# Kernel tuning notes

Hardware: AMD Instinct MI355X
Metric: run time of the kernel (lower is better)

## Reference

```python
import jax, jax.numpy as jnp
import numpy as np

N_NODES = 50000
N_RELS = 50
N_CLASSES = 40
EMB_DIM = 16
RP = 16
N_TRIPLES = 400000


def setup_inputs() -> dict:
    rng = np.random.default_rng(0)
    s = rng.integers(0, N_NODES, size=N_TRIPLES)
    r = rng.integers(0, N_RELS, size=N_TRIPLES)
    o = rng.integers(0, N_NODES, size=N_TRIPLES)
    # unique (s,o) pairs, as in torch.unique(pairs, dim=0, return_inverse=True)
    pairs = np.stack([s, o], axis=1)
    unique_pairs, inverse = np.unique(pairs, axis=0, return_inverse=True)
    nt = unique_pairs.shape[0]
    # relation_matrix COO (nt, num_rels), coalesced (duplicate (row,col) summed)
    keys = inverse.astype(np.int64) * N_RELS + r
    uk, counts = np.unique(keys, return_counts=True)
    rm_rows = (uk // N_RELS).astype(np.int32)
    rm_cols = (uk % N_RELS).astype(np.int32)
    rm_vals = counts.astype(np.float32)
    # hindices / vindices exactly as in __init__ (note o*rm / s*rm construction)
    s_u = unique_pairs[:, 0].astype(np.int64)
    o_u = unique_pairs[:, 1].astype(np.int64)
    rm = np.arange(RP, dtype=np.int64)[:, None]            # (rp, 1)
    h_rows = np.broadcast_to(s_u[None, :], (RP, nt)).reshape(-1).astype(np.int32)
    h_cols = (o_u[None, :] * rm).reshape(-1).astype(np.int32)
    v_rows = (s_u[None, :] * rm).reshape(-1).astype(np.int32)
    v_cols = np.broadcast_to(o_u[None, :], (RP, nt)).reshape(-1).astype(np.int32)
    # float params (xavier-like scale for weights, randn for rel emb, zero biases)
    key = jax.random.key(0)
    k1, k2, k3 = jax.random.split(key, 3)
    gain = np.sqrt(2.0)  # relu gain
    w1_std = gain * np.sqrt(2.0 / (N_NODES + EMB_DIM))
    w2_std = gain * np.sqrt(2.0 / (EMB_DIM + N_CLASSES))
    return {
        'rel_emb': jax.random.normal(k1, (N_RELS, RP), dtype=jnp.float32),
        'weights1': jax.random.normal(k2, (RP, N_NODES, EMB_DIM), dtype=jnp.float32) * w1_std,
        'weights2': jax.random.normal(k3, (RP, EMB_DIM, N_CLASSES), dtype=jnp.float32) * w2_std,
        'bias1': jnp.zeros((EMB_DIM,), dtype=jnp.float32),
        'bias2': jnp.zeros((N_CLASSES,), dtype=jnp.float32),
        'rm_rows': jnp.asarray(rm_rows),
        'rm_cols': jnp.asarray(rm_cols),
        'rm_vals': jnp.asarray(rm_vals),
        'h_rows': jnp.asarray(h_rows),
        'h_cols': jnp.asarray(h_cols),
        'v_rows': jnp.asarray(v_rows),
        'v_cols': jnp.asarray(v_cols),
    }


def reference(rel_emb, weights1, weights2, bias1, bias2,
              rm_rows, rm_cols, rm_vals, h_rows, h_cols, v_rows, v_cols):
    rp, n, e = weights1.shape
    nt = h_rows.shape[0] // rp
    # latents = sparse.mm(relation_matrix, relation_embeddings) -> (nt, rp)
    latents = jax.ops.segment_sum(rm_vals[:, None] * rel_emb[rm_cols], rm_rows,
                                  num_segments=nt)
    latents = jax.nn.softmax(latents, axis=1)
    lf = latents.T.reshape(-1)                              # (rp*nt,)
    # sum_sparse(hindices, lf, (n, n*rp), row=False): per-column sums, gathered
    colsum = jax.ops.segment_sum(lf, h_cols, num_segments=n * rp)
    ln = lf / colsum[h_cols]
    # spmm(hindices, ln, (n, n*rp), weights1_flat) -> (n, e)
    w1f = weights1.reshape(rp * n, e)
    h = jax.ops.segment_sum(ln[:, None] * w1f[h_cols], h_rows, num_segments=n)
    h = jax.nn.relu(h + bias1)
    # sum_sparse(vindices, lf, (n*rp, n), row=True): per-row sums, gathered
    rowsum = jax.ops.segment_sum(lf, v_rows, num_segments=n * rp)
    ln2 = lf / rowsum[v_rows]
    # spmm(vindices, ln2, (n*rp, n), h) -> (n*rp, e)
    h2 = jax.ops.segment_sum(ln2[:, None] * h[v_cols], v_rows, num_segments=n * rp)
    h2 = h2.reshape(rp, n, e)
    out = jnp.einsum('rhc,rnh->nc', weights2, h2) + bias2
    return out
```

## Files before the change

### kernel.cpp

```cpp
#include <hip/hip_runtime.h>

#define RP 16
#define EMB 16
#define NC 40

__global__ void k_latents(const float* __restrict__ rel_emb,
                          const int* __restrict__ rows,
                          const int* __restrict__ cols,
                          const float* __restrict__ vals,
                          float* __restrict__ latents, int nm) {
    int i = blockIdx.x * blockDim.x + threadIdx.x;
    int e = i >> 4, k = i & 15;
    if (e >= nm) return;
    int row = rows[e];
    if (e > 0 && rows[e - 1] == row) return;
    float acc = vals[e] * rel_emb[cols[e] * RP + k];
    while (e + 1 < nm && rows[e + 1] == row) {
        ++e;
        acc += vals[e] * rel_emb[cols[e] * RP + k];
    }
    float m = acc;
    #pragma unroll
    for (int d = 1; d < 16; d <<= 1) m = fmaxf(m, __shfl_xor(m, d, 16));
    float v = expf(acc - m);
    float s = v;
    #pragma unroll
    for (int d = 1; d < 16; d <<= 1) s += __shfl_xor(s, d, 16);
    latents[row * RP + k] = v / s;
}

__global__ void k_r0(const float* __restrict__ latents,
                     float* __restrict__ rowsum, float* __restrict__ colsum,
                     int nt) {
    float acc = 0.f;
    for (int t = blockIdx.x * blockDim.x + threadIdx.x; t < nt;
         t += gridDim.x * blockDim.x)
        acc += latents[t * RP];
    #pragma unroll
    for (int d = 32; d; d >>= 1) acc += __shfl_down(acc, d, 64);
    __shared__ float sm[4];
    int lane = threadIdx.x & 63, wid = threadIdx.x >> 6;
    if (lane == 0) sm[wid] = acc;
    __syncthreads();
    if (threadIdx.x == 0) {
        float tot = sm[0] + sm[1] + sm[2] + sm[3];
        atomicAdd(&rowsum[0], tot);
        atomicAdd(&colsum[0], tot);
    }
}

__global__ void k_count(const int* __restrict__ s_u, const int* __restrict__ o_u,
                        int* __restrict__ cnt_s, int* __restrict__ cnt_o, int nt) {
    int t = blockIdx.x * blockDim.x + threadIdx.x;
    if (t < nt) {
        atomicAdd(&cnt_s[s_u[t]], 1);
        atomicAdd(&cnt_o[o_u[t]], 1);
    }
}

__global__ void k_scan_blk(const int* __restrict__ cnt_s, int* __restrict__ offs_s,
                           const int* __restrict__ cnt_o, int* __restrict__ offs_o,
                           int* __restrict__ partials, int n, int nblk) {
    const int* in = blockIdx.y ? cnt_o : cnt_s;
    int* out = blockIdx.y ? offs_o : offs_s;
    int tid = threadIdx.x;
    int i0 = blockIdx.x * 1024 + tid * 4;
    int v[4];
    #pragma unroll
    for (int q = 0; q < 4; ++q) {
        int i = i0 + q;
        v[q] = (i < n) ? in[i] : 0;
    }
    int tsum = v[0] + v[1] + v[2] + v[3];
    int lane = tid & 63, wid = tid >> 6;
    int x = tsum;
    #pragma unroll
    for (int d = 1; d < 64; d <<= 1) {
        int u = __shfl_up(x, d, 64);
        if (lane >= d) x += u;
    }
    __shared__ int wsum[4];
    if (lane == 63) wsum[wid] = x;
    __syncthreads();
    int woff = 0;
    for (int wq = 0; wq < wid; ++wq) woff += wsum[wq];
    int run = woff + x - tsum;
    #pragma unroll
    for (int q = 0; q < 4; ++q) {
        int i = i0 + q;
        if (i < n) out[i] = run;
        run += v[q];
    }
    if (tid == 255) partials[blockIdx.y * nblk + blockIdx.x] = run;
}

__global__ void k_scan_top(int* __restrict__ partials, int nblk) {
    int w = threadIdx.x >> 6;
    int lane = threadIdx.x & 63;
    int carry = 0;
    for (int base = 0; base < nblk; base += 64) {
        int idx = base + lane;
        int v = (idx < nblk) ? partials[w * nblk + idx] : 0;
        int x = v;
        #pragma unroll
        for (int d = 1; d < 64; d <<= 1) {
            int u = __shfl_up(x, d, 64);
            if (lane >= d) x += u;
        }
        if (idx < nblk) partials[w * nblk + idx] = carry + x - v;
        carry += __shfl(x, 63, 64);
    }
}

__global__ void k_scan_add(int* __restrict__ offs_s, int* __restrict__ cur_s,
                           int* __restrict__ offs_o, int* __restrict__ cur_o,
                           const int* __restrict__ partials, int n, int nblk) {
    int* out = blockIdx.y ? offs_o : offs_s;
    int* cur = blockIdx.y ? cur_o : cur_s;
    int add = partials[blockIdx.y * nblk + blockIdx.x];
    int i0 = blockIdx.x * 1024 + threadIdx.x * 4;
    #pragma unroll
    for (int q = 0; q < 4; ++q) {
        int i = i0 + q;
        if (i < n) {
            int vv = out[i] + add;
            out[i] = vv;
            cur[i] = vv;
        }
    }
}

__global__ void k_scatter(const int* __restrict__ s_u, const int* __restrict__ o_u,
                          int* __restrict__ cur_s, int* __restrict__ cur_o,
                          int* __restrict__ bkt_s, int* __restrict__ bkt_o, int nt) {
    int t = blockIdx.x * blockDim.x + threadIdx.x;
    if (t < nt) {
        bkt_s[atomicAdd(&cur_s[s_u[t]], 1)] = t;
        bkt_o[atomicAdd(&cur_o[o_u[t]], 1)] = t;
    }
}

__global__ void k_latsum(const float* __restrict__ latents,
                         const int* __restrict__ bkt_s,
                         const int* __restrict__ offs_s,
                         const int* __restrict__ cnt_s,
                         float* __restrict__ rowsum,
                         const int* __restrict__ bkt_o,
                         const int* __restrict__ offs_o,
                         const int* __restrict__ cnt_o,
                         float* __restrict__ colsum, int n) {
    const int* bkt  = blockIdx.y ? bkt_o : bkt_s;
    const int* offs = blockIdx.y ? offs_o : offs_s;
    const int* cnt  = blockIdx.y ? cnt_o : cnt_s;
    float* dst      = blockIdx.y ? colsum : rowsum;
    int i = blockIdx.x * blockDim.x + threadIdx.x;
    int v = i >> 4, k = i & 15;
    if (v >= n) return;
    int beg = offs[v], d = cnt[v];
    if (d == 0) return;
    float ls = 0.f;
    for (int j0 = 0; j0 < d; j0 += 16) {
        int tj = bkt[beg + min(j0 + k, d - 1)];
        #pragma unroll
        for (int e = 0; e < 16; ++e) {
            if (j0 + e >= d) break;
            int t = __shfl(tj, e, 16);
            ls += latents[t * RP + k];
        }
    }
    if (k >= 1) atomicAdd(&dst[v * k], ls);
}

__global__ void k_h_acc(const float* __restrict__ latents,
                        const int* __restrict__ bkt_o,
                        const int* __restrict__ offs_o,
                        const int* __restrict__ cnt_o,
                        const int* __restrict__ s_u,
                        const float* __restrict__ colsum,
                        const float* __restrict__ w1,
                        float* __restrict__ h, int n) {
    int i = blockIdx.x * blockDim.x + threadIdx.x;
    int o = i >> 4, k = i & 15;
    if (o >= n) return;
    int d = cnt_o[o];
    if (d == 0) return;
    int beg = offs_o[o];
    float W[RP];
    #pragma unroll
    for (int r = 0; r < RP; ++r)
        W[r] = w1[(size_t)(o * r) * EMB + k];
    float rcp_cs = 1.f / colsum[o * k];
    for (int j0 = 0; j0 < d; j0 += 16) {
        int tj = bkt_o[beg + min(j0 + k, d - 1)];
        int sj = s_u[tj];
        #pragma unroll
        for (int e = 0; e < 16; ++e) {
            if (j0 + e >= d) break;
            int t = __shfl(tj, e, 16);
            float ln = latents[t * RP + k] * rcp_cs;
            float acc = 0.f;
            #pragma unroll
            for (int r = 0; r < RP; ++r)
                acc += __shfl(ln, r, 16) * W[r];
            int s = __shfl(sj, e, 16);
            atomicAdd(&h[s * EMB + k], acc);
        }
    }
}

__global__ void k_h2(const float* __restrict__ latents,
                     const int* __restrict__ bkt_s,
                     const int* __restrict__ offs_s,
                     const int* __restrict__ cnt_s,
                     const int* __restrict__ o_u,
                     const float* __restrict__ rowsum,
                     const float* __restrict__ h,
                     const float* __restrict__ bias1,
                     float* __restrict__ h2,
                     float* __restrict__ r0part, int n) {
    __shared__ float r0acc[EMB];
    if (threadIdx.x < EMB) r0acc[threadIdx.x] = 0.f;
    __syncthreads();
    int i = blockIdx.x * blockDim.x + threadIdx.x;
    int s = i >> 4, k = i & 15;
    float b1k = bias1[k];
    float M[RP];
    #pragma unroll
    for (int r = 0; r < RP; ++r) M[r] = 0.f;
    int d = 0;
    if (s < n) {
        int beg = offs_s[s];
        d = cnt_s[s];
        for (int j0 = 0; j0 < d; j0 += 16) {
            int tj = bkt_s[beg + min(j0 + k, d - 1)];
            int oj = o_u[tj];
            #pragma unroll
            for (int e = 0; e < 16; ++e) {
                if (j0 + e >= d) break;
                int t = __shfl(tj, e, 16);
                int o = __shfl(oj, e, 16);
                float hv = fmaxf(h[o * EMB + k] + b1k, 0.f);
                float lat = latents[t * RP + k];
                #pragma unroll
                for (int r = 0; r < RP; ++r)
                    M[r] += __shfl(lat, r, 16) * hv;
            }
        }
    }
    if (s < n && d > 0) {
        float rs = rowsum[s * k];
        float rs0 = __shfl(rs, 0, 16);
        atomicAdd(&r0acc[k], M[0] / rs0);
        #pragma unroll
        for (int r = 1; r < RP; ++r) {
            float rsr = __shfl(rs, r, 16);
            atomicAdd(&h2[(size_t)(s * r) * EMB + k], M[r] / rsr);
        }
    }
    __syncthreads();
    if (threadIdx.x < EMB)
        r0part[(size_t)blockIdx.x * EMB + threadIdx.x] = r0acc[threadIdx.x];
}

__global__ void k_h2r0(const float* __restrict__ r0part,
                       float* __restrict__ h2, int nblk) {
    __shared__ float red[1024];
    int k = threadIdx.x & 15, j0 = threadIdx.x >> 4;
    float acc = 0.f;
    for (int j = j0; j < nblk; j += 64)
        acc += r0part[(size_t)j * EMB + k];
    red[j0 * 16 + k] = acc;
    __syncthreads();
    #pragma unroll
    for (int st = 32; st >= 1; st >>= 1) {
        if (j0 < st) red[j0 * 16 + k] += red[(j0 + st) * 16 + k];
        __syncthreads();
    }
    if (threadIdx.x < 16) h2[threadIdx.x] += red[threadIdx.x];
}

#define CB2 20
__global__ void k_out(const float* __restrict__ w2,
                      const float* __restrict__ bias2,
                      const float* __restrict__ h2,
                      float* __restrict__ out, int n) {
    __shared__ float w2s[RP * EMB * NC];
    for (int i = threadIdx.x; i < RP * EMB * NC; i += 256)
        w2s[i] = w2[i];
    __syncthreads();
    int gi = blockIdx.x * blockDim.x + threadIdx.x;
    int node = gi >> 1;
    int c0 = (gi & 1) * CB2;
    if (node >= n) return;
    float acc[CB2];
    #pragma unroll
    for (int c = 0; c < CB2; ++c) acc[c] = bias2[c0 + c];
    for (int rq = 0; rq < RP; ++rq) {
        const float4* h2row = (const float4*)&h2[((size_t)rq * n + node) * EMB];
        float4 hv4[4];
        #pragma unroll
        for (int q = 0; q < 4; ++q) hv4[q] = h2row[q];
        const float* hv = (const float*)hv4;
        #pragma unroll
        for (int hh = 0; hh < EMB; ++hh) {
            const float4* wrow = (const float4*)&w2s[(rq * EMB + hh) * NC + c0];
            float hvv = hv[hh];
            #pragma unroll
            for (int q5 = 0; q5 < 5; ++q5) {
                float4 wv = wrow[q5];
                acc[q5 * 4 + 0] += wv.x * hvv;
                acc[q5 * 4 + 1] += wv.y * hvv;
                acc[q5 * 4 + 2] += wv.z * hvv;
                acc[q5 * 4 + 3] += wv.w * hvv;
            }
        }
    }
    float4* op = (float4*)&out[node * NC + c0];
    #pragma unroll
    for (int q5 = 0; q5 < 5; ++q5)
        op[q5] = make_float4(acc[q5 * 4], acc[q5 * 4 + 1],
                             acc[q5 * 4 + 2], acc[q5 * 4 + 3]);
}

extern "C" void kernel_launch(void* const* d_in, const int* in_sizes, int n_in,
                              void* d_out, int out_size, void* d_ws, size_t ws_size,
                              hipStream_t stream) {
    const float* rel_emb = (const float*)d_in[0];
    const float* w1      = (const float*)d_in[1];
    const float* w2      = (const float*)d_in[2];
    const float* b1      = (const float*)d_in[3];
    const float* b2      = (const float*)d_in[4];
    const int*   rm_rows = (const int*)d_in[5];
    const int*   rm_cols = (const int*)d_in[6];
    const float* rm_vals = (const float*)d_in[7];
    const int*   h_rows  = (const int*)d_in[8];
    const int*   v_cols  = (const int*)d_in[11];

    const int nm = in_sizes[5];
    const int ne = in_sizes[8];
    const int nt = ne / RP;
    const int n  = in_sizes[1] / (RP * EMB);

    const int B = 256;
    const int nblk_h2 = (n * 16 + B - 1) / B;
    const int nblk_sc = (n + 1023) / 1024;

    char* w = (char*)d_ws;
    float* colsum = (float*)w;  w += (size_t)n * RP * 4;
    float* rowsum = (float*)w;  w += (size_t)n * RP * 4;
    float* h2     = (float*)w;  w += (size_t)n * RP * EMB * 4;
    float* h      = (float*)w;  w += (size_t)n * EMB * 4;
    int* cnt_s    = (int*)w;    w += (size_t)n * 4;
    int* cnt_o    = (int*)w;    w += (size_t)n * 4;
    size_t zero_bytes = (size_t)(w - (char*)d_ws);
    float* latents = (float*)w; w += (size_t)nt * RP * 4;
    int* offs_s    = (int*)w;   w += (size_t)n * 4;
    int* cur_s     = (int*)w;   w += (size_t)n * 4;
    int* offs_o    = (int*)w;   w += (size_t)n * 4;
    int* cur_o     = (int*)w;   w += (size_t)n * 4;
    int* bkt_s     = (int*)w;   w += (size_t)nt * 4;
    int* bkt_o     = (int*)w;   w += (size_t)nt * 4;
    float* r0part  = (float*)w; w += (size_t)nblk_h2 * EMB * 4;
    int* partials  = (int*)w;   w += (size_t)2 * nblk_sc * 4;
    if ((size_t)(w - (char*)d_ws) > ws_size) return;

    hipMemsetAsync(d_ws, 0, zero_bytes, stream);

    k_latents<<<dim3((nm * 16 + B - 1) / B), dim3(B), 0, stream>>>(
        rel_emb, rm_rows, rm_cols, rm_vals, latents, nm);
    k_r0<<<dim3(64), dim3(B), 0, stream>>>(latents, rowsum, colsum, nt);
    k_count<<<dim3((nt + B - 1) / B), dim3(B), 0, stream>>>(
        h_rows, v_cols, cnt_s, cnt_o, nt);
    k_scan_blk<<<dim3(nblk_sc, 2), dim3(B), 0, stream>>>(
        cnt_s, offs_s, cnt_o, offs_o, partials, n, nblk_sc);
    k_scan_top<<<dim3(1), dim3(128), 0, stream>>>(partials, nblk_sc);
    k_scan_add<<<dim3(nblk_sc, 2), dim3(B), 0, stream>>>(
        offs_s, cur_s, offs_o, cur_o, partials, n, nblk_sc);
    k_scatter<<<dim3((nt + B - 1) / B), dim3(B), 0, stream>>>(
        h_rows, v_cols, cur_s, cur_o, bkt_s, bkt_o, nt);
    k_latsum<<<dim3((n * 16 + B - 1) / B, 2), dim3(B), 0, stream>>>(
        latents, bkt_s, offs_s, cnt_s, rowsum, bkt_o, offs_o, cnt_o, colsum, n);
    k_h_acc<<<dim3((n * 16 + B - 1) / B), dim3(B), 0, stream>>>(
        latents, bkt_o, offs_o, cnt_o, h_rows, colsum, w1, h, n);
    k_h2<<<dim3(nblk_h2), dim3(B), 0, stream>>>(
        latents, bkt_s, offs_s, cnt_s, v_cols, rowsum, h, b1, h2, r0part, n);
    k_h2r0<<<dim3(1), dim3(1024), 0, stream>>>(r0part, h2, nblk_h2);
    k_out<<<dim3((n * 2 + B - 1) / B), dim3(B), 0, stream>>>(
        w2, b2, h2, (float*)d_out, n);
}
```

Baseline: 319.9 us.

## Scatter latents into bucket-sorted copies during softmax, dropping index indirection

The latents kernel now runs after the CSR offsets are built. It writes each softmaxed latent row directly into subject-sorted and object-sorted copies, along with the partner node index. This removes the separate scatter kernel and the bucket-index gather in latsum, h_acc and h2, so those kernels read contiguous rows instead of doing random latents[t] lookups. The cost is twice the latent storage, an extra scattered write per row, and atomic cursor traffic inside the softmax kernel. k_r0 now reads the s-sorted copy, which is a permutation of the same data, so its sum is unchanged.

```diff
diff --git a/kernel.cpp b/kernel.cpp
--- a/kernel.cpp
+++ b/kernel.cpp
@@ -3,12 +3,98 @@
 #define RP 16
 #define EMB 16
 #define NC 40
+
+__global__ void k_count(const int* __restrict__ s_u, const int* __restrict__ o_u,
+                        int* __restrict__ cnt_s, int* __restrict__ cnt_o, int nt) {
+    int t = blockIdx.x * blockDim.x + threadIdx.x;
+    if (t < nt) {
+        atomicAdd(&cnt_s[s_u[t]], 1);
+        atomicAdd(&cnt_o[o_u[t]], 1);
+    }
+}
+
+__global__ void k_scan_blk(const int* __restrict__ cnt_s, int* __restrict__ offs_s,
+                           const int* __restrict__ cnt_o, int* __restrict__ offs_o,
+                           int* __restrict__ partials, int n, int nblk) {
+    const int* in = blockIdx.y ? cnt_o : cnt_s;
+    int* out = blockIdx.y ? offs_o : offs_s;
+    int tid = threadIdx.x;
+    int i0 = blockIdx.x * 1024 + tid * 4;
+    int v[4];
+    #pragma unroll
+    for (int q = 0; q < 4; ++q) {
+        int i = i0 + q;
+        v[q] = (i < n) ? in[i] : 0;
+    }
+    int tsum = v[0] + v[1] + v[2] + v[3];
+    int lane = tid & 63, wid = tid >> 6;
+    int x = tsum;
+    #pragma unroll
+    for (int d = 1; d < 64; d <<= 1) {
+        int u = __shfl_up(x, d, 64);
+        if (lane >= d) x += u;
+    }
+    __shared__ int wsum[4];
+    if (lane == 63) wsum[wid] = x;
+    __syncthreads();
+    int woff = 0;
+    for (int wq = 0; wq < wid; ++wq) woff += wsum[wq];
+    int run = woff + x - tsum;
+    #pragma unroll
+    for (int q = 0; q < 4; ++q) {
+        int i = i0 + q;
+        if (i < n) out[i] = run;
+        run += v[q];
+    }
+    if (tid == 255) partials[blockIdx.y * nblk + blockIdx.x] = run;
+}
+
+__global__ void k_scan_top(int* __restrict__ partials, int nblk) {
+    int w = threadIdx.x >> 6;
+    int lane = threadIdx.x & 63;
+    int carry = 0;
+    for (int base = 0; base < nblk; base += 64) {
+        int idx = base + lane;
+        int v = (idx < nblk) ? partials[w * nblk + idx] : 0;
+        int x = v;
+        #pragma unroll
+        for (int d = 1; d < 64; d <<= 1) {
+            int u = __shfl_up(x, d, 64);
+            if (lane >= d) x += u;
+        }
+        if (idx < nblk) partials[w * nblk + idx] = carry + x - v;
+        carry += __shfl(x, 63, 64);
+    }
+}
+
+__global__ void k_scan_add(int* __restrict__ offs_s, int* __restrict__ cur_s,
+                           int* __restrict__ offs_o, int* __restrict__ cur_o,
+                           const int* __restrict__ partials, int n, int nblk) {
+    int* out = blockIdx.y ? offs_o : offs_s;
+    int* cur = blockIdx.y ? cur_o : cur_s;
+    int add = partials[blockIdx.y * nblk + blockIdx.x];
+    int i0 = blockIdx.x * 1024 + threadIdx.x * 4;
+    #pragma unroll
+    for (int q = 0; q < 4; ++q) {
+        int i = i0 + q;
+        if (i < n) {
+            int vv = out[i] + add;
+            out[i] = vv;
+            cur[i] = vv;
+        }
+    }
+}
 
 __global__ void k_latents(const float* __restrict__ rel_emb,
                           const int* __restrict__ rows,
                           const int* __restrict__ cols,
                           const float* __restrict__ vals,
-                          float* __restrict__ latents, int nm) {
+                          const int* __restrict__ s_u,
+                          const int* __restrict__ o_u,
+                          int* __restrict__ cur_s, int* __restrict__ cur_o,
+                          float* __restrict__ lat_s, float* __restrict__ lat_o,
+                          int* __restrict__ ou_s, int* __restrict__ su_o,
+                          int nm) {
     int i = blockIdx.x * blockDim.x + threadIdx.x;
     int e = i >> 4, k = i & 15;
     if (e >= nm) return;
@@ -26,16 +112,31 @@
     float s = v;
     #pragma unroll
     for (int d = 1; d < 16; d <<= 1) s += __shfl_xor(s, d, 16);
-    latents[row * RP + k] = v / s;
-}
-
-__global__ void k_r0(const float* __restrict__ latents,
+    v = v / s;
+    int ps = 0, po = 0, su = 0, ou = 0;
+    if (k == 0) {
+        su = s_u[row];
+        ou = o_u[row];
+        ps = atomicAdd(&cur_s[su], 1);
+        po = atomicAdd(&cur_o[ou], 1);
+    }
+    ps = __shfl(ps, 0, 16);
+    po = __shfl(po, 0, 16);
+    lat_s[(size_t)ps * RP + k] = v;
+    lat_o[(size_t)po * RP + k] = v;
+    if (k == 0) {
+        ou_s[ps] = ou;
+        su_o[po] = su;
+    }
+}
+
+__global__ void k_r0(const float* __restrict__ lat_s,
                      float* __restrict__ rowsum, float* __restrict__ colsum,
                      int nt) {
     float acc = 0.f;
     for (int t = blockIdx.x * blockDim.x + threadIdx.x; t < nt;
          t += gridDim.x * blockDim.x)
-        acc += latents[t * RP];
+        acc += lat_s[(size_t)t * RP];
     #pragma unroll
     for (int d = 32; d; d >>= 1) acc += __shfl_down(acc, d, 64);
     __shared__ float sm[4];
@@ -49,107 +150,15 @@
     }
 }
 
-__global__ void k_count(const int* __restrict__ s_u, const int* __restrict__ o_u,
-                        int* __restrict__ cnt_s, int* __restrict__ cnt_o, int nt) {
-    int t = blockIdx.x * blockDim.x + threadIdx.x;
-    if (t < nt) {
-        atomicAdd(&cnt_s[s_u[t]], 1);
-        atomicAdd(&cnt_o[o_u[t]], 1);
-    }
-}
-
-__global__ void k_scan_blk(const int* __restrict__ cnt_s, int* __restrict__ offs_s,
-                           const int* __restrict__ cnt_o, int* __restrict__ offs_o,
-                           int* __restrict__ partials, int n, int nblk) {
-    const int* in = blockIdx.y ? cnt_o : cnt_s;
-    int* out = blockIdx.y ? offs_o : offs_s;
-    int tid = threadIdx.x;
-    int i0 = blockIdx.x * 1024 + tid * 4;
-    int v[4];
-    #pragma unroll
-    for (int q = 0; q < 4; ++q) {
-        int i = i0 + q;
-        v[q] = (i < n) ? in[i] : 0;
-    }
-    int tsum = v[0] + v[1] + v[2] + v[3];
-    int lane = tid & 63, wid = tid >> 6;
-    int x = tsum;
-    #pragma unroll
-    for (int d = 1; d < 64; d <<= 1) {
-        int u = __shfl_up(x, d, 64);
-        if (lane >= d) x += u;
-    }
-    __shared__ int wsum[4];
-    if (lane == 63) wsum[wid] = x;
-    __syncthreads();
-    int woff = 0;
-    for (int wq = 0; wq < wid; ++wq) woff += wsum[wq];
-    int run = woff + x - tsum;
-    #pragma unroll
-    for (int q = 0; q < 4; ++q) {
-        int i = i0 + q;
-        if (i < n) out[i] = run;
-        run += v[q];
-    }
-    if (tid == 255) partials[blockIdx.y * nblk + blockIdx.x] = run;
-}
-
-__global__ void k_scan_top(int* __restrict__ partials, int nblk) {
-    int w = threadIdx.x >> 6;
-    int lane = threadIdx.x & 63;
-    int carry = 0;
-    for (int base = 0; base < nblk; base += 64) {
-        int idx = base + lane;
-        int v = (idx < nblk) ? partials[w * nblk + idx] : 0;
-        int x = v;
-        #pragma unroll
-        for (int d = 1; d < 64; d <<= 1) {
-            int u = __shfl_up(x, d, 64);
-            if (lane >= d) x += u;
-        }
-        if (idx < nblk) partials[w * nblk + idx] = carry + x - v;
-        carry += __shfl(x, 63, 64);
-    }
-}
-
-__global__ void k_scan_add(int* __restrict__ offs_s, int* __restrict__ cur_s,
-                           int* __restrict__ offs_o, int* __restrict__ cur_o,
-                           const int* __restrict__ partials, int n, int nblk) {
-    int* out = blockIdx.y ? offs_o : offs_s;
-    int* cur = blockIdx.y ? cur_o : cur_s;
-    int add = partials[blockIdx.y * nblk + blockIdx.x];
-    int i0 = blockIdx.x * 1024 + threadIdx.x * 4;
-    #pragma unroll
-    for (int q = 0; q < 4; ++q) {
-        int i = i0 + q;
-        if (i < n) {
-            int vv = out[i] + add;
-            out[i] = vv;
-            cur[i] = vv;
-        }
-    }
-}
-
-__global__ void k_scatter(const int* __restrict__ s_u, const int* __restrict__ o_u,
-                          int* __restrict__ cur_s, int* __restrict__ cur_o,
-                          int* __restrict__ bkt_s, int* __restrict__ bkt_o, int nt) {
-    int t = blockIdx.x * blockDim.x + threadIdx.x;
-    if (t < nt) {
-        bkt_s[atomicAdd(&cur_s[s_u[t]], 1)] = t;
-        bkt_o[atomicAdd(&cur_o[o_u[t]], 1)] = t;
-    }
-}
-
-__global__ void k_latsum(const float* __restrict__ latents,
-                         const int* __restrict__ bkt_s,
+__global__ void k_latsum(const float* __restrict__ lat_s,
                          const int* __restrict__ offs_s,
                          const int* __restrict__ cnt_s,
                          float* __restrict__ rowsum,
-                         const int* __restrict__ bkt_o,
+                         const float* __restrict__ lat_o,
                          const int* __restrict__ offs_o,
                          const int* __restrict__ cnt_o,
                          float* __restrict__ colsum, int n) {
-    const int* bkt  = blockIdx.y ? bkt_o : bkt_s;
+    const float* lat = blockIdx.y ? lat_o : lat_s;
     const int* offs = blockIdx.y ? offs_o : offs_s;
     const int* cnt  = blockIdx.y ? cnt_o : cnt_s;
     float* dst      = blockIdx.y ? colsum : rowsum;
@@ -159,23 +168,22 @@
     int beg = offs[v], d = cnt[v];
     if (d == 0) return;
     float ls = 0.f;
-    for (int j0 = 0; j0 < d; j0 += 16) {
-        int tj = bkt[beg + min(j0 + k, d - 1)];
-        #pragma unroll
-        for (int e = 0; e < 16; ++e) {
-            if (j0 + e >= d) break;
-            int t = __shfl(tj, e, 16);
-            ls += latents[t * RP + k];
-        }
-    }
+    int j = 0;
+    for (; j + 4 <= d; j += 4) {
+        float a0 = lat[(size_t)(beg + j + 0) * RP + k];
+        float a1 = lat[(size_t)(beg + j + 1) * RP + k];
+        float a2 = lat[(size_t)(beg + j + 2) * RP + k];
+        float a3 = lat[(size_t)(beg + j + 3) * RP + k];
+        ls += (a0 + a1) + (a2 + a3);
+    }
+    for (; j < d; ++j) ls += lat[(size_t)(beg + j) * RP + k];
     if (k >= 1) atomicAdd(&dst[v * k], ls);
 }
 
-__global__ void k_h_acc(const float* __restrict__ latents,
-                        const int* __restrict__ bkt_o,
+__global__ void k_h_acc(const float* __restrict__ lat_o,
                         const int* __restrict__ offs_o,
                         const int* __restrict__ cnt_o,
-                        const int* __restrict__ s_u,
+                        const int* __restrict__ su_o,
                         const float* __restrict__ colsum,
                         const float* __restrict__ w1,
                         float* __restrict__ h, int n) {
@@ -190,29 +198,21 @@
     for (int r = 0; r < RP; ++r)
         W[r] = w1[(size_t)(o * r) * EMB + k];
     float rcp_cs = 1.f / colsum[o * k];
-    for (int j0 = 0; j0 < d; j0 += 16) {
-        int tj = bkt_o[beg + min(j0 + k, d - 1)];
-        int sj = s_u[tj];
-        #pragma unroll
-        for (int e = 0; e < 16; ++e) {
-            if (j0 + e >= d) break;
-            int t = __shfl(tj, e, 16);
-            float ln = latents[t * RP + k] * rcp_cs;
-            float acc = 0.f;
-            #pragma unroll
-            for (int r = 0; r < RP; ++r)
-                acc += __shfl(ln, r, 16) * W[r];
-            int s = __shfl(sj, e, 16);
-            atomicAdd(&h[s * EMB + k], acc);
-        }
-    }
-}
-
-__global__ void k_h2(const float* __restrict__ latents,
-                     const int* __restrict__ bkt_s,
+    for (int j = 0; j < d; ++j) {
+        float ln = lat_o[(size_t)(beg + j) * RP + k] * rcp_cs;
+        int s = su_o[beg + j];
+        float acc = 0.f;
+        #pragma unroll
+        for (int r = 0; r < RP; ++r)
+            acc += __shfl(ln, r, 16) * W[r];
+        atomicAdd(&h[s * EMB + k], acc);
+    }
+}
+
+__global__ void k_h2(const float* __restrict__ lat_s,
                      const int* __restrict__ offs_s,
                      const int* __restrict__ cnt_s,
-                     const int* __restrict__ o_u,
+                     const int* __restrict__ ou_s,
                      const float* __restrict__ rowsum,
                      const float* __restrict__ h,
                      const float* __restrict__ bias1,
@@ -231,20 +231,13 @@
     if (s < n) {
         int beg = offs_s[s];
         d = cnt_s[s];
-        for (int j0 = 0; j0 < d; j0 += 16) {
-            int tj = bkt_s[beg + min(j0 + k, d - 1)];
-            int oj = o_u[tj];
+        for (int j = 0; j < d; ++j) {
+            int o = ou_s[beg + j];
+            float hv = fmaxf(h[o * EMB + k] + b1k, 0.f);
+            float lat = lat_s[(size_t)(beg + j) * RP + k];
             #pragma unroll
-            for (int e = 0; e < 16; ++e) {
-                if (j0 + e >= d) break;
-                int t = __shfl(tj, e, 16);
-                int o = __shfl(oj, e, 16);
-                float hv = fmaxf(h[o * EMB + k] + b1k, 0.f);
-                float lat = latents[t * RP + k];
-                #pragma unroll
-                for (int r = 0; r < RP; ++r)
-                    M[r] += __shfl(lat, r, 16) * hv;
-            }
+            for (int r = 0; r < RP; ++r)
+                M[r] += __shfl(lat, r, 16) * hv;
         }
     }
     if (s < n && d > 0) {
@@ -353,22 +346,20 @@
     int* cnt_s    = (int*)w;    w += (size_t)n * 4;
     int* cnt_o    = (int*)w;    w += (size_t)n * 4;
     size_t zero_bytes = (size_t)(w - (char*)d_ws);
-    float* latents = (float*)w; w += (size_t)nt * RP * 4;
-    int* offs_s    = (int*)w;   w += (size_t)n * 4;
-    int* cur_s     = (int*)w;   w += (size_t)n * 4;
-    int* offs_o    = (int*)w;   w += (size_t)n * 4;
-    int* cur_o     = (int*)w;   w += (size_t)n * 4;
-    int* bkt_s     = (int*)w;   w += (size_t)nt * 4;
-    int* bkt_o     = (int*)w;   w += (size_t)nt * 4;
-    float* r0part  = (float*)w; w += (size_t)nblk_h2 * EMB * 4;
-    int* partials  = (int*)w;   w += (size_t)2 * nblk_sc * 4;
+    float* lat_s  = (float*)w;  w += (size_t)nt * RP * 4;
+    float* lat_o  = (float*)w;  w += (size_t)nt * RP * 4;
+    int* ou_s     = (int*)w;    w += (size_t)nt * 4;
+    int* su_o     = (int*)w;    w += (size_t)nt * 4;
+    int* offs_s   = (int*)w;    w += (size_t)n * 4;
+    int* cur_s    = (int*)w;    w += (size_t)n * 4;
+    int* offs_o   = (int*)w;    w += (size_t)n * 4;
+    int* cur_o    = (int*)w;    w += (size_t)n * 4;
+    float* r0part = (float*)w;  w += (size_t)nblk_h2 * EMB * 4;
+    int* partials = (int*)w;    w += (size_t)2 * nblk_sc * 4;
     if ((size_t)(w - (char*)d_ws) > ws_size) return;
 
     hipMemsetAsync(d_ws, 0, zero_bytes, stream);
 
-    k_latents<<<dim3((nm * 16 + B - 1) / B), dim3(B), 0, stream>>>(
-        rel_emb, rm_rows, rm_cols, rm_vals, latents, nm);
-    k_r0<<<dim3(64), dim3(B), 0, stream>>>(latents, rowsum, colsum, nt);
     k_count<<<dim3((nt + B - 1) / B), dim3(B), 0, stream>>>(
         h_rows, v_cols, cnt_s, cnt_o, nt);
     k_scan_blk<<<dim3(nblk_sc, 2), dim3(B), 0, stream>>>(
@@ -376,14 +367,16 @@
     k_scan_top<<<dim3(1), dim3(128), 0, stream>>>(partials, nblk_sc);
     k_scan_add<<<dim3(nblk_sc, 2), dim3(B), 0, stream>>>(
         offs_s, cur_s, offs_o, cur_o, partials, n, nblk_sc);
-    k_scatter<<<dim3((nt + B - 1) / B), dim3(B), 0, stream>>>(
-        h_rows, v_cols, cur_s, cur_o, bkt_s, bkt_o, nt);
+    k_latents<<<dim3((nm * 16 + B - 1) / B), dim3(B), 0, stream>>>(
+        rel_emb, rm_rows, rm_cols, rm_vals, h_rows, v_cols,
+        cur_s, cur_o, lat_s, lat_o, ou_s, su_o, nm);
+    k_r0<<<dim3(64), dim3(B), 0, stream>>>(lat_s, rowsum, colsum, nt);
     k_latsum<<<dim3((n * 16 + B - 1) / B, 2), dim3(B), 0, stream>>>(
-        latents, bkt_s, offs_s, cnt_s, rowsum, bkt_o, offs_o, cnt_o, colsum, n);
+        lat_s, offs_s, cnt_s, rowsum, lat_o, offs_o, cnt_o, colsum, n);
     k_h_acc<<<dim3((n * 16 + B - 1) / B), dim3(B), 0, stream>>>(
-        latents, bkt_o, offs_o, cnt_o, h_rows, colsum, w1, h, n);
+        lat_o, offs_o, cnt_o, su_o, colsum, w1, h, n);
     k_h2<<<dim3(nblk_h2), dim3(B), 0, stream>>>(
-        latents, bkt_s, offs_s, cnt_s, v_cols, rowsum, h, b1, h2, r0part, n);
+        lat_s, offs_s, cnt_s, ou_s, rowsum, h, b1, h2, r0part, n);
     k_h2r0<<<dim3(1), dim3(1024), 0, stream>>>(r0part, h2, nblk_h2);
     k_out<<<dim3((n * 2 + B - 1) / B), dim3(B), 0, stream>>>(
         w2, b2, h2, (float*)d_out, n);
```

Result: faster. 305.2 us (-4.6%).
